# Kernel tuning notes

Measured on AMD Instinct MI355X. Metric: run time of the kernel, lower is better.

The kernel has to match this reference:

```python
import jax, jax.numpy as jnp
import numpy as np

B, N, DIM, HEADS = 1, 4096, 1024, 16
HEAD_DIM = DIM // HEADS
SCALE = HEAD_DIM ** -0.5
GRID = 64  # GRID*GRID == N, power-of-2 Hilbert grid


def _hilbert_d2xy(n, d):
    # standard Hilbert curve distance->(x,y), vectorized in numpy
    rx = np.zeros_like(d)
    ry = np.zeros_like(d)
    x = np.zeros_like(d)
    y = np.zeros_like(d)
    t = d.copy()
    s = 1
    while s < n:
        rx = (t // 2) & 1
        ry = (t ^ rx) & 1
        # rotate
        swap = ry == 0
        flip = swap & (rx == 1)
        x_f = np.where(flip, s - 1 - x, x)
        y_f = np.where(flip, s - 1 - y, y)
        x, y = np.where(swap, y_f, x_f), np.where(swap, x_f, y_f)
        x = x + s * rx
        y = y + s * ry
        t = t // 4
        s *= 2
    return x, y


def _hilbert_indices(n_tokens, grid):
    d = np.arange(n_tokens)
    hx, hy = _hilbert_d2xy(grid, d)
    # token at Hilbert distance d lives at row-major position hy*grid+hx
    return (hy * grid + hx).astype(np.int32)


def setup_inputs() -> dict:
    key = jax.random.key(0)
    k1, k2, k3 = jax.random.split(key, 3)
    x = jax.random.normal(k1, (B, N, DIM), dtype=jnp.float32)
    w_qkv = jax.random.normal(k2, (3 * DIM, DIM), dtype=jnp.float32) * (DIM ** -0.5)
    w_out = jax.random.normal(k3, (DIM, DIM), dtype=jnp.float32) * (DIM ** -0.5)
    indices = jnp.asarray(_hilbert_indices(N, GRID))
    return {"x": x, "w_qkv": w_qkv, "w_out": w_out, "indices": indices}


def reference(x, w_qkv, w_out, indices):
    b, n, c = x.shape
    # qkv projection: nn.Linear -> x @ W^T, reshape to [B,N,3,H,Dh]
    qkv = jnp.einsum("bnc,dc->bnd", x, w_qkv).reshape(b, n, 3, HEADS, HEAD_DIM)
    q, k, v = qkv[:, :, 0], qkv[:, :, 1], qkv[:, :, 2]  # each [B,N,H,Dh]
    # Hilbert gather along sequence
    q = q[:, indices]
    k = k[:, indices]
    v = v[:, indices]
    # full softmax attention per head
    scores = jnp.einsum("bnhd,bmhd->bhnm", q, k) * SCALE
    attn = jax.nn.softmax(scores, axis=-1)
    out = jnp.einsum("bhnm,bmhd->bnhd", attn, v)  # [B,N,H,Dh]
    # scatter back to original order
    inv = jnp.argsort(indices)
    out = out[:, inv].reshape(b, n, c)
    return jnp.einsum("bnc,dc->bnd", out, w_out)
```

## Files before the change

kernel.cpp:

```cpp
#include <hip/hip_runtime.h>
#include <stdint.h>

#define NTOK 4096
#define HD 64
#define DIMC 1024

typedef __attribute__((ext_vector_type(8))) short s16x8;
typedef __attribute__((ext_vector_type(4))) float f32x4;

#if __has_builtin(__builtin_amdgcn_exp2f)
#define EXP2(x) __builtin_amdgcn_exp2f(x)
#else
#define EXP2(x) exp2f(x)
#endif

__device__ inline unsigned short f2bf(float f) {
  union { float f; unsigned u; } v; v.f = f;
  unsigned r = v.u + 0x7FFFu + ((v.u >> 16) & 1u);
  return (unsigned short)(r >> 16);
}

__device__ inline unsigned cvt_pk_bf16(float lo, float hi) {
  unsigned r;
  asm("v_cvt_pk_bf16_f32 %0, %1, %2" : "=v"(r) : "v"(lo), "v"(hi));
  return r;
}

__device__ inline void gld16(const void* g, void* s) {
  __builtin_amdgcn_global_load_lds((const __attribute__((address_space(1))) void*)g,
                                   (__attribute__((address_space(3))) void*)s, 16, 0, 0);
}

#define N4_X   1048576
#define N4_WQ  786432
#define N4_WO  262144
__global__ void cvt_all(const float4* __restrict__ x, const float4* __restrict__ wq,
                        const float4* __restrict__ wo, ushort4* __restrict__ xb,
                        ushort4* __restrict__ wqb, ushort4* __restrict__ wob) {
  int i = blockIdx.x * 256 + threadIdx.x;
  const float4* s; ushort4* d; int off;
  if (i < N4_X) { s = x; d = xb; off = i; }
  else if (i < N4_X + N4_WQ) { s = wq; d = wqb; off = i - N4_X; }
  else { s = wo; d = wob; off = i - (N4_X + N4_WQ); }
  float4 v = s[off];
  ushort4 o;
  o.x = f2bf(v.x); o.y = f2bf(v.y); o.z = f2bf(v.z); o.w = f2bf(v.w);
  d[off] = o;
}

#define QSCALE 0.18033688011112042f
template<int EPI>
__global__ __launch_bounds__(256) void gemm_bt(
    const unsigned short* __restrict__ A,
    const unsigned short* __restrict__ B,
    float* __restrict__ outf,
    unsigned short* __restrict__ qb,
    unsigned short* __restrict__ kb,
    unsigned short* __restrict__ vtb,
    int K, int Nout)
{
  __shared__ unsigned short As[128 * 32];
  __shared__ unsigned short Bs[128 * 32];
  const int t = threadIdx.x;
  const int l = t & 63;
  const int w = t >> 6;
  const int wr = w >> 1, wc = w & 1;
  const int bm = blockIdx.x, bn = blockIdx.y;

  f32x4 acc[4][4];
#pragma unroll
  for (int m = 0; m < 4; ++m)
#pragma unroll
    for (int n = 0; n < 4; ++n)
#pragma unroll
      for (int r = 0; r < 4; ++r) acc[m][n][r] = 0.f;

  for (int kt = 0; kt < K; kt += 32) {
    __syncthreads();
#pragma unroll
    for (int j = 0; j < 2; ++j) {
      const int o = j * 4096 + t * 16;
      const int row = o >> 6;
      const int cole = (o & 63) >> 1;
      gld16(A + (size_t)(bm * 128 + row) * K + kt + cole, (char*)As + o);
      gld16(B + (size_t)(bn * 128 + row) * K + kt + cole, (char*)Bs + o);
    }
    __syncthreads();
    s16x8 af[4], bfr[4];
    const int cb = (l >> 4) * 16;
#pragma unroll
    for (int m = 0; m < 4; ++m)
      af[m] = *(const s16x8*)((const char*)As + (wr * 64 + m * 16 + (l & 15)) * 64 + cb);
#pragma unroll
    for (int n = 0; n < 4; ++n)
      bfr[n] = *(const s16x8*)((const char*)Bs + (wc * 64 + n * 16 + (l & 15)) * 64 + cb);
#pragma unroll
    for (int m = 0; m < 4; ++m)
#pragma unroll
      for (int n = 0; n < 4; ++n)
        acc[m][n] = __builtin_amdgcn_mfma_f32_16x16x32_bf16(af[m], bfr[n], acc[m][n], 0, 0, 0);
  }

#pragma unroll
  for (int m = 0; m < 4; ++m) {
#pragma unroll
    for (int n = 0; n < 4; ++n) {
#pragma unroll
      for (int r = 0; r < 4; ++r) {
        const int gm = bm * 128 + wr * 64 + m * 16 + (l >> 4) * 4 + r;
        const int gn = bn * 128 + wc * 64 + n * 16 + (l & 15);
        const float val = acc[m][n][r];
        if (EPI == 0) {
          const int part = gn >> 10;
          const int h = (gn >> 6) & 15;
          const int dd = gn & 63;
          if (part == 0)      qb[((size_t)h * NTOK + gm) * HD + dd] = f2bf(val * QSCALE);
          else if (part == 1) kb[((size_t)h * NTOK + gm) * HD + dd] = f2bf(val);
          else                vtb[((size_t)h * HD + dd) * NTOK + gm] = f2bf(val);
        } else {
          outf[(size_t)gm * Nout + gn] = val;
        }
      }
    }
  }
}

__global__ __launch_bounds__(128, 2) void fa_kernel(
    const unsigned short* __restrict__ Q,
    const unsigned short* __restrict__ Kin,
    const unsigned short* __restrict__ Vt,
    unsigned short* __restrict__ O)
{
  __shared__ union SH {
    struct { unsigned short K[2][64 * 64]; unsigned short V[2][64 * 64]; } s;
    unsigned short ot[4][16][72];
  } shm;

  const int t = threadIdx.x, l = t & 63, w = t >> 6;
  const int g = l >> 4, q = l & 15;
  const int wg = blockIdx.x;
  const int h = wg & 15;
  const int bq0 = (wg >> 4) * 64;
  const int q0 = bq0 + w * 32;
  const unsigned short* Qh = Q + (size_t)h * NTOK * HD;
  const unsigned short* Kh = Kin + (size_t)h * NTOK * HD;
  const unsigned short* Vh = Vt + (size_t)h * HD * NTOK;

  int offK[4], offV[4];
#pragma unroll
  for (int j = 0; j < 4; ++j) {
    const int o = j * 2048 + t * 16;
    const int rho = o >> 7;
    const int c = o & 127;
    const int swz = (rho & 7) << 4;
    const int n = (rho & 32) | ((rho & 12) << 1) | ((rho & 16) >> 2) | (rho & 3);
    offK[j] = n * 128 + (c ^ swz);
    offV[j] = rho * (NTOK * 2) + (c ^ swz);
  }

  s16x8 qf[2][2];
#pragma unroll
  for (int rb = 0; rb < 2; ++rb)
#pragma unroll
    for (int tq = 0; tq < 2; ++tq)
      qf[rb][tq] = *(const s16x8*)(Qh + (size_t)(q0 + rb * 16 + q) * HD + tq * 32 + g * 8);

  s16x8 ones;
#pragma unroll
  for (int i = 0; i < 8; ++i) ones[i] = (short)0x3F80;

  f32x4 oacc[2][4], lacc[2];
#pragma unroll
  for (int rb = 0; rb < 2; ++rb) {
#pragma unroll
    for (int db = 0; db < 4; ++db)
#pragma unroll
      for (int r = 0; r < 4; ++r) oacc[rb][db][r] = 0.f;
#pragma unroll
    for (int r = 0; r < 4; ++r) lacc[rb][r] = 0.f;
  }

#pragma unroll
  for (int j = 0; j < 4; ++j) {
    const int o = j * 2048 + t * 16;
    gld16((const char*)Kh + offK[j], (char*)shm.s.K[0] + o);
    gld16((const char*)Vh + offV[j], (char*)shm.s.V[0] + o);
  }
  __syncthreads();

  int cur = 0;
  for (int it = 0; it < NTOK / 64; ++it) {
    if (it + 1 < NTOK / 64) {
      const char* kp = (const char*)Kh + (size_t)(it + 1) * 64 * 128;
      const char* vp = (const char*)Vh + (size_t)(it + 1) * 64 * 2;
#pragma unroll
      for (int j = 0; j < 4; ++j) {
        const int o = j * 2048 + t * 16;
        gld16(kp + offK[j], (char*)shm.s.K[cur ^ 1] + o);
        gld16(vp + offV[j], (char*)shm.s.V[cur ^ 1] + o);
      }
    }

    const char* kbase = (const char*)shm.s.K[cur];
    const char* vbase = (const char*)shm.s.V[cur];

    f32x4 sc[2][4];
    __builtin_amdgcn_s_setprio(1);
#pragma unroll
    for (int kb2 = 0; kb2 < 4; ++kb2) {
      const int row = kb2 * 16 + q;
      const int swz = (row & 7) << 4;
      s16x8 kf0 = *(const s16x8*)(kbase + row * 128 + ((g * 16) ^ swz));
      s16x8 kf1 = *(const s16x8*)(kbase + row * 128 + ((64 + g * 16) ^ swz));
#pragma unroll
      for (int rb = 0; rb < 2; ++rb) {
        f32x4 z = {0.f, 0.f, 0.f, 0.f};
        z = __builtin_amdgcn_mfma_f32_16x16x32_bf16(kf0, qf[rb][0], z, 0, 0, 0);
        sc[rb][kb2] = __builtin_amdgcn_mfma_f32_16x16x32_bf16(kf1, qf[rb][1], z, 0, 0, 0);
      }
    }
    __builtin_amdgcn_s_setprio(0);

    union PU { unsigned u[4]; s16x8 v; } pu[2][2];
#pragma unroll
    for (int rb = 0; rb < 2; ++rb)
#pragma unroll
      for (int h2 = 0; h2 < 2; ++h2) {
        pu[rb][h2].u[0] = cvt_pk_bf16(EXP2(sc[rb][2 * h2][0]), EXP2(sc[rb][2 * h2][1]));
        pu[rb][h2].u[1] = cvt_pk_bf16(EXP2(sc[rb][2 * h2][2]), EXP2(sc[rb][2 * h2][3]));
        pu[rb][h2].u[2] = cvt_pk_bf16(EXP2(sc[rb][2 * h2 + 1][0]), EXP2(sc[rb][2 * h2 + 1][1]));
        pu[rb][h2].u[3] = cvt_pk_bf16(EXP2(sc[rb][2 * h2 + 1][2]), EXP2(sc[rb][2 * h2 + 1][3]));
      }

    __builtin_amdgcn_s_setprio(1);
#pragma unroll
    for (int db = 0; db < 4; ++db) {
      const int row = db * 16 + q;
      const int swz = (row & 7) << 4;
      s16x8 vf0 = *(const s16x8*)(vbase + row * 128 + ((g * 16) ^ swz));
      s16x8 vf1 = *(const s16x8*)(vbase + row * 128 + ((64 + g * 16) ^ swz));
#pragma unroll
      for (int rb = 0; rb < 2; ++rb) {
        oacc[rb][db] = __builtin_amdgcn_mfma_f32_16x16x32_bf16(vf0, pu[rb][0].v, oacc[rb][db], 0, 0, 0);
        oacc[rb][db] = __builtin_amdgcn_mfma_f32_16x16x32_bf16(vf1, pu[rb][1].v, oacc[rb][db], 0, 0, 0);
      }
    }
#pragma unroll
    for (int rb = 0; rb < 2; ++rb) {
      lacc[rb] = __builtin_amdgcn_mfma_f32_16x16x32_bf16(ones, pu[rb][0].v, lacc[rb], 0, 0, 0);
      lacc[rb] = __builtin_amdgcn_mfma_f32_16x16x32_bf16(ones, pu[rb][1].v, lacc[rb], 0, 0, 0);
    }
    __builtin_amdgcn_s_setprio(0);

    __syncthreads();
    cur ^= 1;
  }

  __syncthreads();
#pragma unroll
  for (int rb = 0; rb < 2; ++rb) {
    const float inv = 1.f / lacc[rb][0];
    unsigned short (*otw)[72] = shm.ot[w * 2 + rb];
#pragma unroll
    for (int db = 0; db < 4; ++db)
#pragma unroll
      for (int e = 0; e < 2; ++e) {
        unsigned pr = cvt_pk_bf16(oacc[rb][db][2 * e] * inv, oacc[rb][db][2 * e + 1] * inv);
        *(unsigned*)&otw[q][db * 16 + g * 4 + 2 * e] = pr;
      }
  }
  __syncthreads();
#pragma unroll
  for (int rb = 0; rb < 2; ++rb) {
    const int qr = l >> 2, cc = l & 3;
    const unsigned short* src = &shm.ot[w * 2 + rb][qr][cc * 16];
    s16x8 v0 = *(const s16x8*)src;
    s16x8 v1 = *(const s16x8*)(src + 8);
    const int n = q0 + rb * 16 + qr;
    unsigned short* dst = O + (size_t)n * DIMC + h * HD + cc * 16;
    *(s16x8*)dst = v0;
    *(s16x8*)(dst + 8) = v1;
  }
}

extern "C" void kernel_launch(void* const* d_in, const int* in_sizes, int n_in,
                              void* d_out, int out_size, void* d_ws, size_t ws_size,
                              hipStream_t stream) {
  const float* x    = (const float*)d_in[0];
  const float* wqkv = (const float*)d_in[1];
  const float* wout = (const float*)d_in[2];
  float* out = (float*)d_out;
  char* ws = (char*)d_ws;

  unsigned short* xb    = (unsigned short*)(ws);
  unsigned short* wqkvb = (unsigned short*)(ws + 8388608);
  unsigned short* woutb = (unsigned short*)(ws + 14680064);
  unsigned short* Qb    = (unsigned short*)(ws + 16777216);
  unsigned short* Kb    = (unsigned short*)(ws + 25165824);
  unsigned short* Vtb   = (unsigned short*)(ws + 33554432);
  unsigned short* aob   = (unsigned short*)(ws + 41943040);

  cvt_all<<<8192, 256, 0, stream>>>((const float4*)x, (const float4*)wqkv, (const float4*)wout,
                                    (ushort4*)xb, (ushort4*)wqkvb, (ushort4*)woutb);

  gemm_bt<0><<<dim3(32, 24), 256, 0, stream>>>(xb, wqkvb, nullptr, Qb, Kb, Vtb, 1024, 3072);

  fa_kernel<<<1024, 128, 0, stream>>>(Qb, Kb, Vtb, aob);

  gemm_bt<1><<<dim3(32, 8), 256, 0, stream>>>(aob, woutb, out, nullptr, nullptr, nullptr, 1024, 1024);
}
```

Baseline: 164.4 us.

## Split attention over two key halves with a separate combine kernel

Splits the flash-attention key range into two halves processed by separate blocks, which doubles the grid to 2048 blocks and shrinks the K/V tiles to 32 keys so occupancy can rise to 4 blocks per CU. Each half writes unnormalized bf16 partial outputs and row sums, and a new combine kernel adds them and normalizes. The aim is better CU utilization and latency hiding on a grid that was only 1024 blocks. The cost is extra global traffic for the partials, one more kernel launch, and an added bf16 rounding step on the unnormalized partials. It relies on the existing no-max-subtraction softmax, so the halves need no rescaling.

Result: slower. 167.9 us (+2.1%).

```diff
diff --git a/kernel.cpp b/kernel.cpp
--- a/kernel.cpp
+++ b/kernel.cpp
@@ -24,6 +24,11 @@
   unsigned r;
   asm("v_cvt_pk_bf16_f32 %0, %1, %2" : "=v"(r) : "v"(lo), "v"(hi));
   return r;
+}
+
+__device__ inline float bf2f(unsigned short u) {
+  union { unsigned u; float f; } v; v.u = ((unsigned)u) << 16;
+  return v.f;
 }
 
 __device__ inline void gld16(const void* g, void* s) {
@@ -125,37 +130,38 @@
   }
 }
 
-__global__ __launch_bounds__(128, 2) void fa_kernel(
+__global__ __launch_bounds__(128, 4) void fa_split(
     const unsigned short* __restrict__ Q,
     const unsigned short* __restrict__ Kin,
     const unsigned short* __restrict__ Vt,
-    unsigned short* __restrict__ O)
+    unsigned short* __restrict__ Opart,
+    float* __restrict__ Lpart)
 {
-  __shared__ union SH {
-    struct { unsigned short K[2][64 * 64]; unsigned short V[2][64 * 64]; } s;
-    unsigned short ot[4][16][72];
-  } shm;
+  __shared__ unsigned short Ks[2][32 * 64];
+  __shared__ unsigned short Vs[2][64 * 32];
 
   const int t = threadIdx.x, l = t & 63, w = t >> 6;
   const int g = l >> 4, q = l & 15;
   const int wg = blockIdx.x;
   const int h = wg & 15;
-  const int bq0 = (wg >> 4) * 64;
-  const int q0 = bq0 + w * 32;
+  const int qt = (wg >> 4) & 63;
+  const int half = wg >> 10;
+  const int q0 = qt * 64 + w * 32;
+  const int kbase0 = half * (NTOK / 2);
   const unsigned short* Qh = Q + (size_t)h * NTOK * HD;
   const unsigned short* Kh = Kin + (size_t)h * NTOK * HD;
   const unsigned short* Vh = Vt + (size_t)h * HD * NTOK;
 
-  int offK[4], offV[4];
-#pragma unroll
-  for (int j = 0; j < 4; ++j) {
+  int offK[2], offV[2];
+#pragma unroll
+  for (int j = 0; j < 2; ++j) {
     const int o = j * 2048 + t * 16;
     const int rho = o >> 7;
     const int c = o & 127;
-    const int swz = (rho & 7) << 4;
-    const int n = (rho & 32) | ((rho & 12) << 1) | ((rho & 16) >> 2) | (rho & 3);
-    offK[j] = n * 128 + (c ^ swz);
-    offV[j] = rho * (NTOK * 2) + (c ^ swz);
+    const int n = ((rho & 12) << 1) | ((rho & 16) >> 2) | (rho & 3);
+    offK[j] = n * 128 + (c ^ ((rho & 7) << 4));
+    const int rv = o >> 6;
+    offV[j] = rv * (NTOK * 2) + (o & 63);
   }
 
   s16x8 qf[2][2];
@@ -181,37 +187,38 @@
   }
 
 #pragma unroll
-  for (int j = 0; j < 4; ++j) {
+  for (int j = 0; j < 2; ++j) {
     const int o = j * 2048 + t * 16;
-    gld16((const char*)Kh + offK[j], (char*)shm.s.K[0] + o);
-    gld16((const char*)Vh + offV[j], (char*)shm.s.V[0] + o);
+    gld16((const char*)Kh + (size_t)kbase0 * 128 + offK[j], (char*)Ks[0] + o);
+    gld16((const char*)Vh + (size_t)kbase0 * 2 + offV[j], (char*)Vs[0] + o);
   }
   __syncthreads();
 
   int cur = 0;
-  for (int it = 0; it < NTOK / 64; ++it) {
-    if (it + 1 < NTOK / 64) {
-      const char* kp = (const char*)Kh + (size_t)(it + 1) * 64 * 128;
-      const char* vp = (const char*)Vh + (size_t)(it + 1) * 64 * 2;
-#pragma unroll
-      for (int j = 0; j < 4; ++j) {
+  const int NIT = (NTOK / 2) / 32;
+  for (int it = 0; it < NIT; ++it) {
+    if (it + 1 < NIT) {
+      const char* kp = (const char*)Kh + (size_t)(kbase0 + (it + 1) * 32) * 128;
+      const char* vp = (const char*)Vh + (size_t)(kbase0 + (it + 1) * 32) * 2;
+#pragma unroll
+      for (int j = 0; j < 2; ++j) {
         const int o = j * 2048 + t * 16;
-        gld16(kp + offK[j], (char*)shm.s.K[cur ^ 1] + o);
-        gld16(vp + offV[j], (char*)shm.s.V[cur ^ 1] + o);
+        gld16(kp + offK[j], (char*)Ks[cur ^ 1] + o);
+        gld16(vp + offV[j], (char*)Vs[cur ^ 1] + o);
       }
     }
 
-    const char* kbase = (const char*)shm.s.K[cur];
-    const char* vbase = (const char*)shm.s.V[cur];
-
-    f32x4 sc[2][4];
+    const char* kb = (const char*)Ks[cur];
+    const char* vb = (const char*)Vs[cur];
+
+    f32x4 sc[2][2];
     __builtin_amdgcn_s_setprio(1);
 #pragma unroll
-    for (int kb2 = 0; kb2 < 4; ++kb2) {
+    for (int kb2 = 0; kb2 < 2; ++kb2) {
       const int row = kb2 * 16 + q;
       const int swz = (row & 7) << 4;
-      s16x8 kf0 = *(const s16x8*)(kbase + row * 128 + ((g * 16) ^ swz));
-      s16x8 kf1 = *(const s16x8*)(kbase + row * 128 + ((64 + g * 16) ^ swz));
+      s16x8 kf0 = *(const s16x8*)(kb + row * 128 + ((g * 16) ^ swz));
+      s16x8 kf1 = *(const s16x8*)(kb + row * 128 + ((64 + g * 16) ^ swz));
 #pragma unroll
       for (int rb = 0; rb < 2; ++rb) {
         f32x4 z = {0.f, 0.f, 0.f, 0.f};
@@ -221,66 +228,68 @@
     }
     __builtin_amdgcn_s_setprio(0);
 
-    union PU { unsigned u[4]; s16x8 v; } pu[2][2];
-#pragma unroll
-    for (int rb = 0; rb < 2; ++rb)
-#pragma unroll
-      for (int h2 = 0; h2 < 2; ++h2) {
-        pu[rb][h2].u[0] = cvt_pk_bf16(EXP2(sc[rb][2 * h2][0]), EXP2(sc[rb][2 * h2][1]));
-        pu[rb][h2].u[1] = cvt_pk_bf16(EXP2(sc[rb][2 * h2][2]), EXP2(sc[rb][2 * h2][3]));
-        pu[rb][h2].u[2] = cvt_pk_bf16(EXP2(sc[rb][2 * h2 + 1][0]), EXP2(sc[rb][2 * h2 + 1][1]));
-        pu[rb][h2].u[3] = cvt_pk_bf16(EXP2(sc[rb][2 * h2 + 1][2]), EXP2(sc[rb][2 * h2 + 1][3]));
-      }
+    union PU { unsigned u[4]; s16x8 v; } pu[2];
+#pragma unroll
+    for (int rb = 0; rb < 2; ++rb) {
+      pu[rb].u[0] = cvt_pk_bf16(EXP2(sc[rb][0][0]), EXP2(sc[rb][0][1]));
+      pu[rb].u[1] = cvt_pk_bf16(EXP2(sc[rb][0][2]), EXP2(sc[rb][0][3]));
+      pu[rb].u[2] = cvt_pk_bf16(EXP2(sc[rb][1][0]), EXP2(sc[rb][1][1]));
+      pu[rb].u[3] = cvt_pk_bf16(EXP2(sc[rb][1][2]), EXP2(sc[rb][1][3]));
+    }
 
     __builtin_amdgcn_s_setprio(1);
 #pragma unroll
     for (int db = 0; db < 4; ++db) {
       const int row = db * 16 + q;
-      const int swz = (row & 7) << 4;
-      s16x8 vf0 = *(const s16x8*)(vbase + row * 128 + ((g * 16) ^ swz));
-      s16x8 vf1 = *(const s16x8*)(vbase + row * 128 + ((64 + g * 16) ^ swz));
-#pragma unroll
-      for (int rb = 0; rb < 2; ++rb) {
-        oacc[rb][db] = __builtin_amdgcn_mfma_f32_16x16x32_bf16(vf0, pu[rb][0].v, oacc[rb][db], 0, 0, 0);
-        oacc[rb][db] = __builtin_amdgcn_mfma_f32_16x16x32_bf16(vf1, pu[rb][1].v, oacc[rb][db], 0, 0, 0);
-      }
-    }
-#pragma unroll
-    for (int rb = 0; rb < 2; ++rb) {
-      lacc[rb] = __builtin_amdgcn_mfma_f32_16x16x32_bf16(ones, pu[rb][0].v, lacc[rb], 0, 0, 0);
-      lacc[rb] = __builtin_amdgcn_mfma_f32_16x16x32_bf16(ones, pu[rb][1].v, lacc[rb], 0, 0, 0);
-    }
+      s16x8 vf = *(const s16x8*)(vb + row * 64 + g * 16);
+#pragma unroll
+      for (int rb = 0; rb < 2; ++rb)
+        oacc[rb][db] = __builtin_amdgcn_mfma_f32_16x16x32_bf16(vf, pu[rb].v, oacc[rb][db], 0, 0, 0);
+    }
+#pragma unroll
+    for (int rb = 0; rb < 2; ++rb)
+      lacc[rb] = __builtin_amdgcn_mfma_f32_16x16x32_bf16(ones, pu[rb].v, lacc[rb], 0, 0, 0);
     __builtin_amdgcn_s_setprio(0);
 
     __syncthreads();
     cur ^= 1;
   }
 
-  __syncthreads();
+  const size_t pbase = ((size_t)(half * 16 + h) * NTOK);
 #pragma unroll
   for (int rb = 0; rb < 2; ++rb) {
-    const float inv = 1.f / lacc[rb][0];
-    unsigned short (*otw)[72] = shm.ot[w * 2 + rb];
-#pragma unroll
-    for (int db = 0; db < 4; ++db)
-#pragma unroll
-      for (int e = 0; e < 2; ++e) {
-        unsigned pr = cvt_pk_bf16(oacc[rb][db][2 * e] * inv, oacc[rb][db][2 * e + 1] * inv);
-        *(unsigned*)&otw[q][db * 16 + g * 4 + 2 * e] = pr;
-      }
-  }
-  __syncthreads();
-#pragma unroll
-  for (int rb = 0; rb < 2; ++rb) {
-    const int qr = l >> 2, cc = l & 3;
-    const unsigned short* src = &shm.ot[w * 2 + rb][qr][cc * 16];
-    s16x8 v0 = *(const s16x8*)src;
-    s16x8 v1 = *(const s16x8*)(src + 8);
-    const int n = q0 + rb * 16 + qr;
-    unsigned short* dst = O + (size_t)n * DIMC + h * HD + cc * 16;
-    *(s16x8*)dst = v0;
-    *(s16x8*)(dst + 8) = v1;
-  }
+    const int nn = q0 + rb * 16 + q;
+#pragma unroll
+    for (int db = 0; db < 4; ++db) {
+      uint2 pr;
+      pr.x = cvt_pk_bf16(oacc[rb][db][0], oacc[rb][db][1]);
+      pr.y = cvt_pk_bf16(oacc[rb][db][2], oacc[rb][db][3]);
+      *(uint2*)(Opart + (pbase + nn) * HD + db * 16 + g * 4) = pr;
+    }
+    if (g == 0) Lpart[pbase + nn] = lacc[rb][0];
+  }
+}
+
+__global__ __launch_bounds__(256) void fa_combine(
+    const unsigned short* __restrict__ Opart,
+    const float* __restrict__ Lpart,
+    unsigned short* __restrict__ O)
+{
+  const int tid = blockIdx.x * 256 + threadIdx.x;
+  const int d4 = tid & 15;
+  const int n = (tid >> 4) & 4095;
+  const int h = tid >> 16;
+  const size_t e0 = ((size_t)h * NTOK + n) * HD + d4 * 4;
+  const size_t e1 = e0 + (size_t)16 * NTOK * HD;
+  ushort4 a = *(const ushort4*)(Opart + e0);
+  ushort4 b = *(const ushort4*)(Opart + e1);
+  const float inv = 1.f / (Lpart[(size_t)h * NTOK + n] + Lpart[(size_t)(16 + h) * NTOK + n]);
+  ushort4 o;
+  o.x = f2bf((bf2f(a.x) + bf2f(b.x)) * inv);
+  o.y = f2bf((bf2f(a.y) + bf2f(b.y)) * inv);
+  o.z = f2bf((bf2f(a.z) + bf2f(b.z)) * inv);
+  o.w = f2bf((bf2f(a.w) + bf2f(b.w)) * inv);
+  *(ushort4*)(O + (size_t)n * DIMC + h * HD + d4 * 4) = o;
 }
 
 extern "C" void kernel_launch(void* const* d_in, const int* in_sizes, int n_in,
@@ -294,18 +303,22 @@
 
   unsigned short* xb    = (unsigned short*)(ws);
   unsigned short* wqkvb = (unsigned short*)(ws + 8388608);
-  unsigned short* woutb = (unsigned short*)(ws + 14680064);
   unsigned short* Qb    = (unsigned short*)(ws + 16777216);
   unsigned short* Kb    = (unsigned short*)(ws + 25165824);
   unsigned short* Vtb   = (unsigned short*)(ws + 33554432);
   unsigned short* aob   = (unsigned short*)(ws + 41943040);
+  unsigned short* woutb = (unsigned short*)(ws + 50331648);
+  float*          Lp    = (float*)(ws + 52428800);
+  unsigned short* Opart = (unsigned short*)(ws);
 
   cvt_all<<<8192, 256, 0, stream>>>((const float4*)x, (const float4*)wqkv, (const float4*)wout,
                                     (ushort4*)xb, (ushort4*)wqkvb, (ushort4*)woutb);
 
   gemm_bt<0><<<dim3(32, 24), 256, 0, stream>>>(xb, wqkvb, nullptr, Qb, Kb, Vtb, 1024, 3072);
 
-  fa_kernel<<<1024, 128, 0, stream>>>(Qb, Kb, Vtb, aob);
+  fa_split<<<2048, 128, 0, stream>>>(Qb, Kb, Vtb, Opart, Lp);
+
+  fa_combine<<<4096, 256, 0, stream>>>(Opart, Lp, aob);
 
   gemm_bt<1><<<dim3(32, 8), 256, 0, stream>>>(aob, woutb, out, nullptr, nullptr, nullptr, 1024, 1024);
 }
```
